# Optimization experiments

Hardware: AMD Instinct MI355X
Metric: run time of the kernel (lower is better)

## Reference

```python
import jax, jax.numpy as jnp
import numpy as np
from jax import lax

B, S, D, H, W = 4, 4096, 512, 8, 32
LL, LG = 4, 3
HD = D // H
SF = 4   # sparsity_factor
K = 7    # depthwise conv kernel


def _ln(x, g, b):
    mu = x.mean(-1, keepdims=True)
    v = ((x - mu) ** 2).mean(-1, keepdims=True)
    return (x - mu) * lax.rsqrt(v + 1e-5) * g + b


def _mha(x, wqkv, bqkv, wp, bp, bias=None):
    Bx, Sx, Dx = x.shape
    qkv = (x @ wqkv + bqkv).reshape(Bx, Sx, 3, H, HD)
    q, k, v = jnp.moveaxis(qkv, 2, 0)          # each [B,S,H,hd]
    att = jnp.einsum('bqhd,bkhd->bhqk', q, k) * (HD ** -0.5)
    if bias is not None:
        att = att + bias                        # relative position bias [1,H,W,W]
    a = jax.nn.softmax(att, axis=-1)
    o = jnp.einsum('bhqk,bkhd->bqhd', a, v).reshape(Bx, Sx, Dx)
    return o @ wp + bp


def _ffn(x, w1, b1, w2, b2):
    return jax.nn.gelu(x @ w1 + b1) @ w2 + b2


def _dwconv(x, w, b):
    # x [B,S,D], w [D,K] depthwise, 'same' padding
    y = lax.conv_general_dilated(
        x.transpose(0, 2, 1), w[:, None, :], (1,), [((K - 1) // 2, (K - 1) // 2)],
        feature_group_count=D, dimension_numbers=('NCH', 'OIH', 'NCH'))
    return (y + b[:, None]).transpose(0, 2, 1)


def _lin_interp(x, L_out):
    # torch F.interpolate(mode='linear', align_corners=False); x [B,Lin,D]
    Lin = x.shape[1]
    pos = jnp.clip((jnp.arange(L_out, dtype=jnp.float32) + 0.5) * (Lin / L_out) - 0.5,
                   0.0, Lin - 1)
    i0 = jnp.floor(pos).astype(jnp.int32)
    i1 = jnp.minimum(i0 + 1, Lin - 1)
    w = (pos - i0)[None, :, None]
    return x[:, i0] * (1.0 - w) + x[:, i1] * w


_rel_idx = np.arange(W)[:, None] - np.arange(W)[None, :] + W - 1   # [W,W]


def _local_attn(x, wqkv, bqkv, wp, bp, rel):
    # Swin-style non-overlapping window attention with relative position bias
    NW = S // W
    bias = rel[_rel_idx].transpose(2, 0, 1)[None]   # [1,H,W,W]
    xw = x.reshape(B * NW, W, D)
    return _mha(xw, wqkv, bqkv, wp, bp, bias).reshape(B, S, D)


def _global_attn(x, wqkv, bqkv, wp, bp):
    # strided sparse global attention + linear interpolation back to S
    if S > SF * 32:
        stride = max(1, S // (SF * 32))
        xs = x[:, ::stride]                         # [B, 128, D]
        return _lin_interp(_mha(xs, wqkv, bqkv, wp, bp), S)
    return _mha(x, wqkv, bqkv, wp, bp)


def _forward(x, p):
    (lqkv_w, lqkv_b, lproj_w, lproj_b, lrel, lconv_w, lconv_b,
     ln1_g, ln1_b, lffn_w1, lffn_b1, lffn_w2, lffn_b2, ln2_g, ln2_b,
     gqkv_w, gqkv_b, gproj_w, gproj_b, gn1_g, gn1_b,
     gffn_w1, gffn_b1, gffn_w2, gffn_b2, gn2_g, gn2_b,
     fw_local, fw_global, fn_g, fn_b) = p
    # local branch: window attention + depthwise conv + FFN, pre-sum/post-norm
    xl = x
    for i in range(LL):
        a = _local_attn(xl, lqkv_w[i], lqkv_b[i], lproj_w[i], lproj_b[i], lrel[i])
        xl = _ln(xl + a, ln1_g[i], ln1_b[i])
        xl = xl + _dwconv(xl, lconv_w[i], lconv_b[i])
        f = _ffn(xl, lffn_w1[i], lffn_b1[i], lffn_w2[i], lffn_b2[i])
        xl = _ln(xl + f, ln2_g[i], ln2_b[i])
    # global branch: sparse strided attention + FFN
    xg = x
    for i in range(LG):
        a = _global_attn(xg, gqkv_w[i], gqkv_b[i], gproj_w[i], gproj_b[i])
        xg = _ln(xg + a, gn1_g[i], gn1_b[i])
        f = _ffn(xg, gffn_w1[i], gffn_b1[i], gffn_w2[i], gffn_b2[i])
        xg = _ln(xg + f, gn2_g[i], gn2_b[i])
    # weighted_sum branch fusion + LayerNorm
    w = jax.nn.softmax(jnp.stack([fw_local, fw_global]))
    return _ln(w[0] * xl + w[1] * xg, fn_g, fn_b)


def setup_inputs() -> dict:
    ks = iter(jax.random.split(jax.random.key(0), 48))
    def r(shape, s=0.02):
        return jax.random.normal(next(ks), shape, dtype=jnp.float32) * s
    return {
        'x': jax.random.normal(next(ks), (B, S, D), dtype=jnp.float32),
        'lqkv_w': r((LL, D, 3 * D)), 'lqkv_b': jnp.zeros((LL, 3 * D)),
        'lproj_w': r((LL, D, D)), 'lproj_b': jnp.zeros((LL, D)),
        'lrel': r((LL, 2 * W - 1, H)),
        'lconv_w': r((LL, D, K)), 'lconv_b': jnp.zeros((LL, D)),
        'ln1_g': jnp.ones((LL, D)), 'ln1_b': jnp.zeros((LL, D)),
        'lffn_w1': r((LL, D, 4 * D)), 'lffn_b1': jnp.zeros((LL, 4 * D)),
        'lffn_w2': r((LL, 4 * D, D)), 'lffn_b2': jnp.zeros((LL, D)),
        'ln2_g': jnp.ones((LL, D)), 'ln2_b': jnp.zeros((LL, D)),
        'gqkv_w': r((LG, D, 3 * D)), 'gqkv_b': jnp.zeros((LG, 3 * D)),
        'gproj_w': r((LG, D, D)), 'gproj_b': jnp.zeros((LG, D)),
        'gn1_g': jnp.ones((LG, D)), 'gn1_b': jnp.zeros((LG, D)),
        'gffn_w1': r((LG, D, 4 * D)), 'gffn_b1': jnp.zeros((LG, 4 * D)),
        'gffn_w2': r((LG, 4 * D, D)), 'gffn_b2': jnp.zeros((LG, D)),
        'gn2_g': jnp.ones((LG, D)), 'gn2_b': jnp.zeros((LG, D)),
        'fw_local': jnp.float32(0.5), 'fw_global': jnp.float32(0.5),
        'fn_g': jnp.ones((D,)), 'fn_b': jnp.zeros((D,)),
    }


def reference(x, lqkv_w, lqkv_b, lproj_w, lproj_b, lrel, lconv_w, lconv_b,
              ln1_g, ln1_b, lffn_w1, lffn_b1, lffn_w2, lffn_b2, ln2_g, ln2_b,
              gqkv_w, gqkv_b, gproj_w, gproj_b, gn1_g, gn1_b,
              gffn_w1, gffn_b1, gffn_w2, gffn_b2, gn2_g, gn2_b,
              fw_local, fw_global, fn_g, fn_b):
    return _forward(x, (lqkv_w, lqkv_b, lproj_w, lproj_b, lrel, lconv_w, lconv_b,
                        ln1_g, ln1_b, lffn_w1, lffn_b1, lffn_w2, lffn_b2, ln2_g, ln2_b,
                        gqkv_w, gqkv_b, gproj_w, gproj_b, gn1_g, gn1_b,
                        gffn_w1, gffn_b1, gffn_w2, gffn_b2, gn2_g, gn2_b,
                        fw_local, fw_global, fn_g, fn_b))
```

## Files before the change

kernel.cpp:

```cpp
#include <hip/hip_runtime.h>
#include <hip/hip_bf16.h>
#include <math.h>

typedef __attribute__((ext_vector_type(8))) short short8;
typedef __attribute__((ext_vector_type(4))) float float4_t;
typedef __attribute__((ext_vector_type(4))) unsigned int uint4_t;
typedef __attribute__((ext_vector_type(2))) unsigned int uint2_t;

#define DEV static __device__ __forceinline__

DEV unsigned short f2b(float f) {
    union { float f; unsigned int u; } x; x.f = f;
    unsigned int r = x.u + 0x7fffu + ((x.u >> 16) & 1u);
    return (unsigned short)(r >> 16);
}
DEV float b2f(unsigned short u) {
    union { unsigned int u; float f; } x; x.u = ((unsigned int)u) << 16;
    return x.f;
}
DEV unsigned int f2b2(float lo, float hi) {
    union { __hip_bfloat162 h; unsigned int u; } c;
    c.h = __float22bfloat162_rn(make_float2(lo, hi));
    return c.u;
}
DEV float gelu_f(float x) {
    const float a = -2.3022082f, b = -0.10294372f;
    float x2 = x * x;
    float p = __builtin_fmaf(x2, b, a);
    float e = __builtin_amdgcn_exp2f(p * x);
    return x * __builtin_amdgcn_rcpf(1.0f + e);
}

DEV void gld16(unsigned short* lds, const unsigned short* g) {
    __builtin_amdgcn_global_load_lds(
        (const __attribute__((address_space(1))) unsigned int*)g,
        (__attribute__((address_space(3))) unsigned int*)lds,
        16, 0, 0);
}

__global__ __launch_bounds__(256) void transpose_cast_batch_kernel(
    const float* __restrict__ srcL, const float* __restrict__ srcG, int nl,
    unsigned short* __restrict__ dst0, size_t perL, int Kd, int Nd)
{
    const int z = blockIdx.z;
    const float* W = (z < nl) ? srcL + (size_t)z * Kd * Nd
                              : srcG + (size_t)(z - nl) * Kd * Nd;
    unsigned short* WT = dst0 + (size_t)z * perL;
    __shared__ float tile[32][33];
    int n0 = blockIdx.x * 32, k0 = blockIdx.y * 32;
    int tx = threadIdx.x & 31, ty = threadIdx.x >> 5;
    #pragma unroll
    for (int r = ty; r < 32; r += 8)
        tile[r][tx] = W[(size_t)(k0 + r) * Nd + n0 + tx];
    __syncthreads();
    #pragma unroll
    for (int r = ty; r < 32; r += 8)
        WT[(size_t)(n0 + r) * Kd + k0 + tx] = f2b(tile[tx][r]);
}

__global__ __launch_bounds__(256) void copy_cast_kernel(
    const float* __restrict__ x, float* __restrict__ xl, float* __restrict__ xg,
    unsigned short* __restrict__ xb, int n4)
{
    int i = blockIdx.x * 256 + threadIdx.x;
    if (i < n4) {
        float4_t v = ((const float4_t*)x)[i];
        ((float4_t*)xl)[i] = v;
        ((float4_t*)xg)[i] = v;
        uint2_t p = { f2b2(v[0], v[1]), f2b2(v[2], v[3]) };
        ((uint2_t*)xb)[i] = p;
    }
}

template<int BN>
__global__ __launch_bounds__(256, 3) void gemm_db_kernel(
    const unsigned short* __restrict__ A,
    const unsigned short* __restrict__ BT,
    const float* __restrict__ bias,
    const float* __restrict__ residual,
    float* __restrict__ Cf,
    unsigned short* __restrict__ Cb,
    int M, int N, int K, int act)
{
    constexpr int NI = (BN == 128) ? 4 : 2;
    __shared__ __align__(16) unsigned short As[2][128 * 32];
    __shared__ __align__(16) unsigned short Bs[2][BN * 32];
    const int tid = threadIdx.x;
    const int wave = tid >> 6, lane = tid & 63;
    const int quad = lane >> 4, l16 = lane & 15;
    const int m0 = blockIdx.x * 128, n0 = blockIdx.y * BN;
    const int wm = (BN == 128) ? (wave >> 1) * 64 : wave * 32;
    const int wn = (BN == 128) ? (wave & 1) * 64 : 0;

    float4_t acc[NI][4] = {};

    const int lrow = lane >> 2;
    const int lcol = (lane & 3) * 8;
    const int r0 = wave * 16 + lrow;
    const unsigned short* Ag0 = A  + (size_t)(m0 + r0) * K + lcol;
    const unsigned short* Ag1 = A  + (size_t)(m0 + 64 + r0) * K + lcol;
    const unsigned short* Bg0 = BT + (size_t)(n0 + r0) * K + lcol;
    const unsigned short* Bg1 = (BN == 128) ? BT + (size_t)(n0 + 64 + r0) * K + lcol : nullptr;
    const int soff = (wave * 16) * 32 + lane * 8;

    const int iters = K >> 5;
    gld16(&As[0][soff], Ag0);
    gld16(&As[0][soff + 64 * 32], Ag1);
    gld16(&Bs[0][soff], Bg0);
    if (BN == 128) gld16(&Bs[0][soff + 64 * 32], Bg1);
    __syncthreads();

    for (int k = 0; k < iters; k++) {
        const int cur = k & 1;
        if (k + 1 < iters) {
            const int koff = (k + 1) << 5;
            const int nxt = cur ^ 1;
            gld16(&As[nxt][soff], Ag0 + koff);
            gld16(&As[nxt][soff + 64 * 32], Ag1 + koff);
            gld16(&Bs[nxt][soff], Bg0 + koff);
            if (BN == 128) gld16(&Bs[nxt][soff + 64 * 32], Bg1 + koff);
        }
        short8 a[NI], b[4];
        #pragma unroll
        for (int i = 0; i < NI; i++)
            a[i] = *(const short8*)(&As[cur][(wm + i * 16 + l16) * 32 + quad * 8]);
        #pragma unroll
        for (int j = 0; j < 4; j++)
            b[j] = *(const short8*)(&Bs[cur][(wn + j * 16 + l16) * 32 + quad * 8]);
        #pragma unroll
        for (int i = 0; i < NI; i++)
            #pragma unroll
            for (int j = 0; j < 4; j++)
                acc[i][j] = __builtin_amdgcn_mfma_f32_16x16x32_bf16(b[j], a[i], acc[i][j], 0, 0, 0);
        __syncthreads();
    }

    #pragma unroll
    for (int i = 0; i < NI; i++) {
        const int row = m0 + wm + i * 16 + l16;
        #pragma unroll
        for (int j = 0; j < 4; j++) {
            const int col = n0 + wn + j * 16 + quad * 4;
            const size_t idx = (size_t)row * N + col;
            float4_t v = acc[i][j] + *(const float4_t*)(bias + col);
            if (act == 1) {
                #pragma unroll
                for (int r = 0; r < 4; r++) v[r] = gelu_f(v[r]);
            }
            if (residual) v += *(const float4_t*)(residual + idx);
            if (Cf) *(float4_t*)(Cf + idx) = v;
            if (Cb) {
                uint2_t o = { f2b2(v[0], v[1]), f2b2(v[2], v[3]) };
                *(uint2_t*)(Cb + idx) = o;
            }
        }
    }
}

__global__ __launch_bounds__(256) void ln_kernel(
    const float* __restrict__ X, const float* __restrict__ g, const float* __restrict__ b,
    float* __restrict__ Yf, unsigned short* __restrict__ Yb)
{
    const int row = blockIdx.x * 4 + (threadIdx.x >> 6);
    const int lane = threadIdx.x & 63;
    const float* xr = X + (size_t)row * 512 + lane * 8;
    float4_t v0 = *(const float4_t*)(xr);
    float4_t v1 = *(const float4_t*)(xr + 4);
    float s = v0[0] + v0[1] + v0[2] + v0[3] + v1[0] + v1[1] + v1[2] + v1[3];
    #pragma unroll
    for (int m = 32; m > 0; m >>= 1) s += __shfl_xor(s, m);
    float mu = s * (1.0f / 512.0f);
    float4_t d0 = v0 - mu, d1 = v1 - mu;
    float s2 = d0[0]*d0[0] + d0[1]*d0[1] + d0[2]*d0[2] + d0[3]*d0[3]
             + d1[0]*d1[0] + d1[1]*d1[1] + d1[2]*d1[2] + d1[3]*d1[3];
    #pragma unroll
    for (int m = 32; m > 0; m >>= 1) s2 += __shfl_xor(s2, m);
    float rs = rsqrtf(s2 * (1.0f / 512.0f) + 1e-5f);
    float4_t g0 = *(const float4_t*)(g + lane * 8);
    float4_t g1 = *(const float4_t*)(g + lane * 8 + 4);
    float4_t b0 = *(const float4_t*)(b + lane * 8);
    float4_t b1 = *(const float4_t*)(b + lane * 8 + 4);
    float4_t y0 = d0 * rs * g0 + b0;
    float4_t y1 = d1 * rs * g1 + b1;
    if (Yf) {
        float* yr = Yf + (size_t)row * 512 + lane * 8;
        *(float4_t*)(yr) = y0;
        *(float4_t*)(yr + 4) = y1;
    }
    if (Yb) {
        uint4_t pk = { f2b2(y0[0], y0[1]), f2b2(y0[2], y0[3]),
                       f2b2(y1[0], y1[1]), f2b2(y1[2], y1[3]) };
        *(uint4_t*)(Yb + (size_t)row * 512 + lane * 8) = pk;
    }
}

__global__ __launch_bounds__(256) void interp_ln_kernel(
    const float* __restrict__ GA, float* __restrict__ XG,
    const float* __restrict__ g, const float* __restrict__ b,
    unsigned short* __restrict__ Yb)
{
    const int row = blockIdx.x * 4 + (threadIdx.x >> 6);
    const int lane = threadIdx.x & 63;
    const int bb = row >> 12, sfull = row & 4095;
    float pos = (sfull + 0.5f) * (128.0f / 4096.0f) - 0.5f;
    pos = fminf(fmaxf(pos, 0.0f), 127.0f);
    int i0 = (int)floorf(pos);
    int i1 = min(i0 + 1, 127);
    float w = pos - (float)i0;
    const float* ga0 = GA + ((size_t)bb * 128 + i0) * 512 + lane * 8;
    const float* ga1 = GA + ((size_t)bb * 128 + i1) * 512 + lane * 8;
    float* xr = XG + (size_t)row * 512 + lane * 8;
    float4_t v0 = *(const float4_t*)(xr)     + *(const float4_t*)(ga0)     * (1.0f - w) + *(const float4_t*)(ga1)     * w;
    float4_t v1 = *(const float4_t*)(xr + 4) + *(const float4_t*)(ga0 + 4) * (1.0f - w) + *(const float4_t*)(ga1 + 4) * w;
    float s = v0[0] + v0[1] + v0[2] + v0[3] + v1[0] + v1[1] + v1[2] + v1[3];
    #pragma unroll
    for (int m = 32; m > 0; m >>= 1) s += __shfl_xor(s, m);
    float mu = s * (1.0f / 512.0f);
    float4_t d0 = v0 - mu, d1 = v1 - mu;
    float s2 = d0[0]*d0[0] + d0[1]*d0[1] + d0[2]*d0[2] + d0[3]*d0[3]
             + d1[0]*d1[0] + d1[1]*d1[1] + d1[2]*d1[2] + d1[3]*d1[3];
    #pragma unroll
    for (int m = 32; m > 0; m >>= 1) s2 += __shfl_xor(s2, m);
    float rs = rsqrtf(s2 * (1.0f / 512.0f) + 1e-5f);
    float4_t g0 = *(const float4_t*)(g + lane * 8);
    float4_t g1 = *(const float4_t*)(g + lane * 8 + 4);
    float4_t b0 = *(const float4_t*)(b + lane * 8);
    float4_t b1 = *(const float4_t*)(b + lane * 8 + 4);
    float4_t y0 = d0 * rs * g0 + b0;
    float4_t y1 = d1 * rs * g1 + b1;
    *(float4_t*)(xr) = y0;
    *(float4_t*)(xr + 4) = y1;
    uint4_t pk = { f2b2(y0[0], y0[1]), f2b2(y0[2], y0[3]),
                   f2b2(y1[0], y1[1]), f2b2(y1[2], y1[3]) };
    *(uint4_t*)(Yb + (size_t)row * 512 + lane * 8) = pk;
}

__global__ __launch_bounds__(256) void local_attn_kernel(
    const unsigned short* __restrict__ QKV, const float* __restrict__ rel,
    unsigned short* __restrict__ OUT)
{
    const int blk = blockIdx.x;
    const int h = blk & 7;
    const int win = (blk >> 3) & 127;
    const int b = blk >> 10;
    const int rowbase = b * 4096 + win * 32;
    __shared__ float q[32][64], k[32][65], v[32][64];
    __shared__ float sc[32][33];
    const int tid = threadIdx.x;
    const int i = tid >> 3, c = tid & 7;
    {
        const unsigned short* base = QKV + (size_t)(rowbase + i) * 1536 + h * 64 + c * 8;
        short8 qv = *(const short8*)(base);
        short8 kv = *(const short8*)(base + 512);
        short8 vv = *(const short8*)(base + 1024);
        #pragma unroll
        for (int r = 0; r < 8; r++) {
            q[i][c * 8 + r] = b2f((unsigned short)qv[r]);
            k[i][c * 8 + r] = b2f((unsigned short)kv[r]);
            v[i][c * 8 + r] = b2f((unsigned short)vv[r]);
        }
    }
    __syncthreads();
    #pragma unroll
    for (int p = 0; p < 4; p++) {
        int idx = tid + p * 256;
        int si = idx >> 5, sj = idx & 31;
        float s = 0.f;
        #pragma unroll
        for (int d = 0; d < 64; d++) s += q[si][d] * k[sj][d];
        sc[si][sj] = s * 0.125f + rel[(si - sj + 31) * 8 + h];
    }
    __syncthreads();
    {
        const int j0 = c * 4;
        float a0 = sc[i][j0], a1 = sc[i][j0 + 1], a2 = sc[i][j0 + 2], a3 = sc[i][j0 + 3];
        float mx = fmaxf(fmaxf(a0, a1), fmaxf(a2, a3));
        #pragma unroll
        for (int m = 1; m < 8; m <<= 1) mx = fmaxf(mx, __shfl_xor(mx, m));
        float e0 = __expf(a0 - mx), e1 = __expf(a1 - mx), e2 = __expf(a2 - mx), e3 = __expf(a3 - mx);
        float sum = e0 + e1 + e2 + e3;
        #pragma unroll
        for (int m = 1; m < 8; m <<= 1) sum += __shfl_xor(sum, m);
        float inv = 1.0f / sum;
        sc[i][j0] = e0 * inv; sc[i][j0 + 1] = e1 * inv; sc[i][j0 + 2] = e2 * inv; sc[i][j0 + 3] = e3 * inv;
    }
    __syncthreads();
    float o[8] = {};
    #pragma unroll
    for (int j = 0; j < 32; j++) {
        float a = sc[i][j];
        #pragma unroll
        for (int r = 0; r < 8; r++) o[r] += a * v[j][c * 8 + r];
    }
    uint4_t pk = { f2b2(o[0], o[1]), f2b2(o[2], o[3]), f2b2(o[4], o[5]), f2b2(o[6], o[7]) };
    *(uint4_t*)(OUT + (size_t)(rowbase + i) * 512 + h * 64 + c * 8) = pk;
}

__global__ __launch_bounds__(256) void gather_xs_kernel(
    const float* __restrict__ XG, unsigned short* __restrict__ XSB)
{
    int i = blockIdx.x * 256 + threadIdx.x;
    if (i < 65536) {
        int dv = (i & 127) * 4, t = (i >> 7) & 127, b = i >> 14;
        float4_t v = *(const float4_t*)(XG + ((size_t)b * 4096 + t * 32) * 512 + dv);
        uint2_t p = { f2b2(v[0], v[1]), f2b2(v[2], v[3]) };
        *(uint2_t*)(XSB + (size_t)i * 4) = p;
    }
}

__global__ __launch_bounds__(256) void global_attn_kernel(
    const unsigned short* __restrict__ GQKV, unsigned short* __restrict__ GOUT)
{
    const int blk = blockIdx.x;
    const int qt = blk & 3, h = (blk >> 2) & 7, b = blk >> 5;
    __shared__ unsigned short ks[128 * 64], vs[128 * 64];
    __shared__ float qs[32 * 64];
    __shared__ float sc[32 * 128];
    const int tid = threadIdx.x;
    for (int idx = tid; idx < 128 * 64; idx += 256) {
        int j = idx >> 6, d = idx & 63;
        const unsigned short* rowp = GQKV + (size_t)(b * 128 + j) * 1536 + h * 64 + d;
        ks[idx] = rowp[512];
        vs[idx] = rowp[1024];
    }
    for (int idx = tid; idx < 32 * 64; idx += 256) {
        int i = idx >> 6, d = idx & 63;
        qs[idx] = b2f(GQKV[(size_t)(b * 128 + qt * 32 + i) * 1536 + h * 64 + d]);
    }
    __syncthreads();
    for (int idx = tid; idx < 32 * 128; idx += 256) {
        int i = idx >> 7, j = idx & 127;
        float s = 0.f;
        #pragma unroll
        for (int d = 0; d < 64; d++) s += qs[i * 64 + d] * b2f(ks[j * 64 + d]);
        sc[idx] = s * 0.125f;
    }
    __syncthreads();
    if (tid < 32) {
        float mx = -1e30f;
        for (int j = 0; j < 128; j++) mx = fmaxf(mx, sc[tid * 128 + j]);
        float sum = 0.f;
        for (int j = 0; j < 128; j++) { float e = __expf(sc[tid * 128 + j] - mx); sc[tid * 128 + j] = e; sum += e; }
        float inv = 1.0f / sum;
        for (int j = 0; j < 128; j++) sc[tid * 128 + j] *= inv;
    }
    __syncthreads();
    for (int idx = tid; idx < 32 * 64; idx += 256) {
        int i = idx >> 6, d = idx & 63;
        float o = 0.f;
        for (int j = 0; j < 128; j++) o += sc[i * 128 + j] * b2f(vs[j * 64 + d]);
        GOUT[(size_t)(b * 128 + qt * 32 + i) * 512 + h * 64 + d] = f2b(o);
    }
}

__global__ __launch_bounds__(256) void dwconv_add_kernel(
    const float* __restrict__ X, const float* __restrict__ wconv, const float* __restrict__ bconv,
    float* __restrict__ Yf, unsigned short* __restrict__ Yb)
{
    __shared__ float wT[7][512];
    const int tid = threadIdx.x;
    for (int idx = tid; idx < 3584; idx += 256) {
        int d = idx / 7, t = idx - d * 7;
        wT[t][d] = wconv[idx];
    }
    __syncthreads();
    const int b = blockIdx.y;
    const int s0 = blockIdx.x * 16 + (tid >> 7) * 8;
    const int dv = (tid & 127) * 4;
    const float* Xb = X + ((size_t)b * 4096) * 512 + dv;

    float4_t win[14];
    #pragma unroll
    for (int j = 0; j < 14; j++) {
        int ss = s0 - 3 + j;
        win[j] = (ss >= 0 && ss < 4096) ? *(const float4_t*)(Xb + (size_t)ss * 512)
                                        : (float4_t){0.f, 0.f, 0.f, 0.f};
    }
    float4_t bias = *(const float4_t*)(bconv + dv);
    float4_t w[7];
    #pragma unroll
    for (int t = 0; t < 7; t++) w[t] = *(const float4_t*)(&wT[t][dv]);

    #pragma unroll
    for (int j = 0; j < 8; j++) {
        float4_t acc = bias;
        #pragma unroll
        for (int t = 0; t < 7; t++) acc += win[j + t] * w[t];
        float4_t v = win[j + 3] + acc;
        size_t e = ((size_t)b * 4096 + s0 + j) * 512 + dv;
        *(float4_t*)(Yf + e) = v;
        uint2_t o = { f2b2(v[0], v[1]), f2b2(v[2], v[3]) };
        *(uint2_t*)(Yb + e) = o;
    }
}

__global__ __launch_bounds__(256) void final_kernel(
    const float* __restrict__ XL, const float* __restrict__ XG,
    const float* __restrict__ fwl, const float* __restrict__ fwg,
    const float* __restrict__ g, const float* __restrict__ bb, float* __restrict__ out)
{
    const int row = blockIdx.x * 4 + (threadIdx.x >> 6);
    const int lane = threadIdx.x & 63;
    float a = fwl[0], cc = fwg[0];
    float m = fmaxf(a, cc);
    float ea = __expf(a - m), ec = __expf(cc - m);
    float w0 = ea / (ea + ec), w1 = ec / (ea + ec);
    const float* xlr = XL + (size_t)row * 512 + lane * 8;
    const float* xgr = XG + (size_t)row * 512 + lane * 8;
    float4_t v0 = *(const float4_t*)(xlr)     * w0 + *(const float4_t*)(xgr)     * w1;
    float4_t v1 = *(const float4_t*)(xlr + 4) * w0 + *(const float4_t*)(xgr + 4) * w1;
    float s = v0[0] + v0[1] + v0[2] + v0[3] + v1[0] + v1[1] + v1[2] + v1[3];
    #pragma unroll
    for (int mm = 32; mm > 0; mm >>= 1) s += __shfl_xor(s, mm);
    float mu = s * (1.0f / 512.0f);
    float4_t d0 = v0 - mu, d1 = v1 - mu;
    float s2 = d0[0]*d0[0] + d0[1]*d0[1] + d0[2]*d0[2] + d0[3]*d0[3]
             + d1[0]*d1[0] + d1[1]*d1[1] + d1[2]*d1[2] + d1[3]*d1[3];
    #pragma unroll
    for (int mm = 32; mm > 0; mm >>= 1) s2 += __shfl_xor(s2, mm);
    float rs = rsqrtf(s2 * (1.0f / 512.0f) + 1e-5f);
    float4_t g0 = *(const float4_t*)(g + lane * 8);
    float4_t g1 = *(const float4_t*)(g + lane * 8 + 4);
    float4_t b0 = *(const float4_t*)(bb + lane * 8);
    float4_t b1 = *(const float4_t*)(bb + lane * 8 + 4);
    float* orow = out + (size_t)row * 512 + lane * 8;
    *(float4_t*)(orow)     = d0 * rs * g0 + b0;
    *(float4_t*)(orow + 4) = d1 * rs * g1 + b1;
}

extern "C" void kernel_launch(void* const* d_in, const int* in_sizes, int n_in,
                              void* d_out, int out_size, void* d_ws, size_t ws_size,
                              hipStream_t stream)
{
    (void)in_sizes; (void)n_in; (void)out_size; (void)ws_size;
    const float* x       = (const float*)d_in[0];
    const float* lqkv_w  = (const float*)d_in[1];
    const float* lqkv_b  = (const float*)d_in[2];
    const float* lproj_w = (const float*)d_in[3];
    const float* lproj_b = (const float*)d_in[4];
    const float* lrel    = (const float*)d_in[5];
    const float* lconv_w = (const float*)d_in[6];
    const float* lconv_b = (const float*)d_in[7];
    const float* ln1_g   = (const float*)d_in[8];
    const float* ln1_b   = (const float*)d_in[9];
    const float* lffn_w1 = (const float*)d_in[10];
    const float* lffn_b1 = (const float*)d_in[11];
    const float* lffn_w2 = (const float*)d_in[12];
    const float* lffn_b2 = (const float*)d_in[13];
    const float* ln2_g   = (const float*)d_in[14];
    const float* ln2_b   = (const float*)d_in[15];
    const float* gqkv_w  = (const float*)d_in[16];
    const float* gqkv_b  = (const float*)d_in[17];
    const float* gproj_w = (const float*)d_in[18];
    const float* gproj_b = (const float*)d_in[19];
    const float* gn1_g   = (const float*)d_in[20];
    const float* gn1_b   = (const float*)d_in[21];
    const float* gffn_w1 = (const float*)d_in[22];
    const float* gffn_b1 = (const float*)d_in[23];
    const float* gffn_w2 = (const float*)d_in[24];
    const float* gffn_b2 = (const float*)d_in[25];
    const float* gn2_g   = (const float*)d_in[26];
    const float* gn2_b   = (const float*)d_in[27];
    const float* fw_local  = (const float*)d_in[28];
    const float* fw_global = (const float*)d_in[29];
    const float* fn_g    = (const float*)d_in[30];
    const float* fn_b    = (const float*)d_in[31];
    float* out = (float*)d_out;

    const int Btot = 4 * 4096;
    const int nel = Btot * 512;

    char* wsb = (char*)d_ws;
    size_t off = 0;
    auto alloc = [&](size_t bytes) -> void* {
        void* p = wsb + off;
        off = (off + bytes + 255) & ~(size_t)255;
        return p;
    };
    float*          XL   = (float*)alloc((size_t)nel * 4);
    float*          XG   = (float*)alloc((size_t)nel * 4);
    float*          TMP  = (float*)alloc((size_t)nel * 4);
    unsigned short* XBl  = (unsigned short*)alloc((size_t)nel * 2);
    unsigned short* XBg  = (unsigned short*)alloc((size_t)nel * 2);
    unsigned short* AOUT = (unsigned short*)alloc((size_t)nel * 2);
    unsigned short* BIG  = (unsigned short*)alloc((size_t)Btot * 2048 * 2);
    unsigned short* WT   = (unsigned short*)alloc((size_t)22020096 * 2);
    unsigned short* XSB  = (unsigned short*)alloc((size_t)512 * 512 * 2);
    unsigned short* GQKV = (unsigned short*)alloc((size_t)512 * 1536 * 2);
    unsigned short* GOUT = (unsigned short*)alloc((size_t)512 * 512 * 2);
    float*          GA   = (float*)alloc((size_t)512 * 512 * 4);

    const size_t perL = 3145728;
    {
        dim3 blk(256);
        transpose_cast_batch_kernel<<<dim3(1536/32, 512/32, 7), blk, 0, stream>>>(
            lqkv_w, gqkv_w, 4, WT, perL, 512, 1536);
        transpose_cast_batch_kernel<<<dim3(512/32, 512/32, 7), blk, 0, stream>>>(
            lproj_w, gproj_w, 4, WT + 786432, perL, 512, 512);
        transpose_cast_batch_kernel<<<dim3(2048/32, 512/32, 7), blk, 0, stream>>>(
            lffn_w1, gffn_w1, 4, WT + 786432 + 262144, perL, 512, 2048);
        transpose_cast_batch_kernel<<<dim3(512/32, 2048/32, 7), blk, 0, stream>>>(
            lffn_w2, gffn_w2, 4, WT + 786432 + 262144 + 1048576, perL, 2048, 512);
    }

    copy_cast_kernel<<<dim3(nel / 1024), dim3(256), 0, stream>>>(x, XL, XG, XBl, nel / 4);

    auto gemm = [&](const unsigned short* A_, const unsigned short* BT_, const float* bias_,
                    const float* res_, float* Cf_, unsigned short* Cb_,
                    int M_, int N_, int K_, int act_) {
        if (N_ >= 1024) {
            dim3 g(M_ / 128, N_ / 128);
            gemm_db_kernel<128><<<g, dim3(256), 0, stream>>>(A_, BT_, bias_, res_, Cf_, Cb_, M_, N_, K_, act_);
        } else {
            dim3 g(M_ / 128, N_ / 64);
            gemm_db_kernel<64><<<g, dim3(256), 0, stream>>>(A_, BT_, bias_, res_, Cf_, Cb_, M_, N_, K_, act_);
        }
    };

    for (int i = 0; i < 4; i++) {
        unsigned short* base  = WT + (size_t)i * perL;
        unsigned short* qkvT  = base;
        unsigned short* projT = base + 786432;
        unsigned short* w1T   = base + 786432 + 262144;
        unsigned short* w2T   = base + 786432 + 262144 + 1048576;

        gemm(XBl, qkvT, lqkv_b + i * 1536, nullptr, nullptr, BIG, Btot, 1536, 512, 0);
        local_attn_kernel<<<dim3(4096), dim3(256), 0, stream>>>(BIG, lrel + (size_t)i * 63 * 8, AOUT);
        gemm(AOUT, projT, lproj_b + i * 512, XL, TMP, nullptr, Btot, 512, 512, 0);
        ln_kernel<<<dim3(Btot / 4), dim3(256), 0, stream>>>(TMP, ln1_g + i * 512, ln1_b + i * 512, XL, (unsigned short*)nullptr);
        dwconv_add_kernel<<<dim3(256, 4), dim3(256), 0, stream>>>(XL, lconv_w + (size_t)i * 512 * 7, lconv_b + i * 512, TMP, XBl);
        gemm(XBl, w1T, lffn_b1 + i * 2048, nullptr, nullptr, BIG, Btot, 2048, 512, 1);
        gemm(BIG, w2T, lffn_b2 + i * 512, TMP, TMP, nullptr, Btot, 512, 2048, 0);
        ln_kernel<<<dim3(Btot / 4), dim3(256), 0, stream>>>(TMP, ln2_g + i * 512, ln2_b + i * 512, XL, XBl);
    }

    for (int i = 0; i < 3; i++) {
        unsigned short* base  = WT + (size_t)(4 + i) * perL;
        unsigned short* qkvT  = base;
        unsigned short* projT = base + 786432;
        unsigned short* w1T   = base + 786432 + 262144;
        unsigned short* w2T   = base + 786432 + 262144 + 1048576;

        gather_xs_kernel<<<dim3(256), dim3(256), 0, stream>>>(XG, XSB);
        gemm(XSB, qkvT, gqkv_b + i * 1536, nullptr, nullptr, GQKV, 512, 1536, 512, 0);
        global_attn_kernel<<<dim3(128), dim3(256), 0, stream>>>(GQKV, GOUT);
        gemm(GOUT, projT, gproj_b + i * 512, nullptr, GA, nullptr, 512, 512, 512, 0);
        interp_ln_kernel<<<dim3(Btot / 4), dim3(256), 0, stream>>>(GA, XG, gn1_g + i * 512, gn1_b + i * 512, XBg);
        gemm(XBg, w1T, gffn_b1 + i * 2048, nullptr, nullptr, BIG, Btot, 2048, 512, 1);
        gemm(BIG, w2T, gffn_b2 + i * 512, XG, TMP, nullptr, Btot, 512, 2048, 0);
        ln_kernel<<<dim3(Btot / 4), dim3(256), 0, stream>>>(TMP, gn2_g + i * 512, gn2_b + i * 512, XG, XBg);
    }

    final_kernel<<<dim3(Btot / 4), dim3(256), 0, stream>>>(XL, XG, fw_local, fw_global, fn_g, fn_b, out);
}
```

Measured before the change: 1.943 ms.

## Add 512-thread 256-row GEMM with interleaved LDS/MFMA phases and prefetch

Adds a new bf16 MFMA GEMM kernel with 256xBN block tiles and 8 waves. Each K step is split into four phases that interleave LDS fragment reads, MFMA quarters and asynchronous global-to-LDS staging for step t+2, using explicit vmcnt/lgkmcnt waits, barriers and setprio. The dispatcher sends the large-M GEMMs to this kernel. The goal is to raise per-block data reuse and overlap memory traffic with matrix math. The cost is heavier register and LDS use (about 128KB LDS, acc 8xNJ) and many barriers that may limit occupancy.

```diff
diff --git a/kernel.cpp b/kernel.cpp
--- a/kernel.cpp
+++ b/kernel.cpp
@@ -156,6 +156,160 @@
         }
     }
 }
+
+
+#define BAR __builtin_amdgcn_s_barrier()
+#define LGKM0 asm volatile("s_waitcnt lgkmcnt(0)" ::: "memory")
+#define VMC8 asm volatile("s_waitcnt vmcnt(8)" ::: "memory")
+#define VMC6 asm volatile("s_waitcnt vmcnt(6)" ::: "memory")
+#define VMC0 asm volatile("s_waitcnt vmcnt(0)" ::: "memory")
+#define VMLP do { if constexpr (BN == 256) { VMC8; } else { VMC6; } } while (0)
+
+#define DSA(d, rh) do { \
+    const unsigned short* s_ = &AS[d][wm][0]; \
+    _Pragma("unroll") \
+    for (int ii = 0; ii < 4; ++ii) { \
+        const int row_ = ((rh) * 4 + ii) * 16 + l16; \
+        const int sw_ = (row_ & 7) << 3; \
+        a[ii][0] = *(const short8*)(s_ + row_ * 64 + ((quad * 8) ^ sw_)); \
+        a[ii][1] = *(const short8*)(s_ + row_ * 64 + ((32 + quad * 8) ^ sw_)); \
+    } } while (0)
+
+#define DSB(d, ch) do { \
+    const unsigned short* s_ = &BS[d][wn >> 1][0]; \
+    _Pragma("unroll") \
+    for (int jj = 0; jj < NJH; ++jj) { \
+        const int row_ = wnb + ((ch) * NJH + jj) * 16 + l16; \
+        const int sw_ = (row_ & 7) << 3; \
+        b[(ch) * NJH + jj][0] = *(const short8*)(s_ + row_ * 64 + ((quad * 8) ^ sw_)); \
+        b[(ch) * NJH + jj][1] = *(const short8*)(s_ + row_ * 64 + ((32 + quad * 8) ^ sw_)); \
+    } } while (0)
+
+#define MFMAQ(rh, ch) do { \
+    __builtin_amdgcn_s_setprio(1); \
+    _Pragma("unroll") \
+    for (int ii = 0; ii < 4; ++ii) { \
+        _Pragma("unroll") \
+        for (int jj = 0; jj < NJH; ++jj) { \
+            acc[(rh)*4+ii][(ch)*NJH+jj] = __builtin_amdgcn_mfma_f32_16x16x32_bf16( \
+                b[(ch)*NJH+jj][0], a[ii][0], acc[(rh)*4+ii][(ch)*NJH+jj], 0, 0, 0); \
+            acc[(rh)*4+ii][(ch)*NJH+jj] = __builtin_amdgcn_mfma_f32_16x16x32_bf16( \
+                b[(ch)*NJH+jj][1], a[ii][1], acc[(rh)*4+ii][(ch)*NJH+jj], 0, 0, 0); \
+        } } \
+    __builtin_amdgcn_s_setprio(0); } while (0)
+
+#define KSTEP(d, t, DOSTAGE, VMOP) do { \
+     \
+    DSA(d, 0); DSB(d, 0); BAR; LGKM0; MFMAQ(0, 0); BAR; \
+     \
+    DSB(d, 1); BAR; LGKM0; MFMAQ(0, 1); BAR; \
+     \
+    DSA(d, 1); if (DOSTAGE) { stageB(d, (t) + 2); } BAR; LGKM0; MFMAQ(1, 0); BAR; \
+     \
+    if (DOSTAGE) { stageA(d, (t) + 2); } VMOP; BAR; MFMAQ(1, 1); BAR; \
+  } while (0)
+
+template<int BN>
+__global__ __launch_bounds__(512, 2) void gemm_8ph_kernel(
+    const unsigned short* __restrict__ A,
+    const unsigned short* __restrict__ BT,
+    const float* __restrict__ bias,
+    const float* __restrict__ residual,
+    float* __restrict__ Cf,
+    unsigned short* __restrict__ Cb,
+    int M, int N, int K, int act)
+{
+    static_assert(BN == 256 || BN == 128, "BN");
+    constexpr int NJ  = BN / 64;
+    constexpr int NJH = NJ / 2;
+    constexpr int HB  = BN / 2;
+    constexpr int BLH = (BN == 256) ? 2 : 1;
+
+    __shared__ __align__(16) unsigned short AS[2][2][128 * 64];
+    __shared__ __align__(16) unsigned short BS[2][2][HB * 64];
+
+    const int tid = threadIdx.x;
+    const int wave = tid >> 6, lane = tid & 63;
+    const int quad = lane >> 4, l16 = lane & 15;
+    const int wm = wave >> 2;
+    const int wn = wave & 3;
+    const int m0 = blockIdx.x * 256, n0 = blockIdx.y * BN;
+    const int wnb = (wn & 1) * (BN / 4);
+
+    const int trow = tid >> 3;
+    const int xo = (((tid & 7) ^ (trow & 7)) << 3);
+
+    const unsigned short* gA[2][2];
+    #pragma unroll
+    for (int h = 0; h < 2; ++h)
+        #pragma unroll
+        for (int l = 0; l < 2; ++l)
+            gA[h][l] = A + (size_t)(m0 + h * 128 + l * 64 + trow) * K + xo;
+    const unsigned short* gB[2][BLH];
+    #pragma unroll
+    for (int h = 0; h < 2; ++h)
+        #pragma unroll
+        for (int l = 0; l < BLH; ++l)
+            gB[h][l] = BT + (size_t)(n0 + h * HB + l * 64 + trow) * K + xo;
+
+    auto stageA = [&](int d, int t) {
+        #pragma unroll
+        for (int h = 0; h < 2; ++h)
+            #pragma unroll
+            for (int l = 0; l < 2; ++l)
+                gld16(&AS[d][h][l * 4096 + tid * 8], gA[h][l] + t * 64);
+    };
+    auto stageB = [&](int d, int t) {
+        #pragma unroll
+        for (int h = 0; h < 2; ++h)
+            #pragma unroll
+            for (int l = 0; l < BLH; ++l)
+                gld16(&BS[d][h][l * 4096 + tid * 8], gB[h][l] + t * 64);
+    };
+
+    short8 a[4][2];
+    short8 b[NJ][2];
+    float4_t acc[8][NJ] = {};
+
+    const int T = K >> 6;
+
+    stageA(0, 0); stageB(0, 0);
+    stageA(1, 1); stageB(1, 1);
+    VMLP; BAR;
+
+    for (int t = 0; t < T - 2; ++t) {
+        const int d = t & 1;
+        KSTEP(d, t, true, VMLP);
+    }
+    KSTEP((T - 2) & 1, T - 2, false, VMC0);
+    KSTEP((T - 1) & 1, T - 1, false, (void)0);
+
+    #pragma unroll
+    for (int i = 0; i < 8; ++i) {
+        const int row = m0 + wm * 128 + i * 16 + l16;
+        #pragma unroll
+        for (int j = 0; j < NJ; ++j) {
+            const int col = n0 + (wn >> 1) * HB + wnb + j * 16 + quad * 4;
+            const size_t idx = (size_t)row * N + col;
+            float4_t v = acc[i][j] + *(const float4_t*)(bias + col);
+            if (act == 1) {
+                #pragma unroll
+                for (int r = 0; r < 4; r++) v[r] = gelu_f(v[r]);
+            }
+            if (residual) v += *(const float4_t*)(residual + idx);
+            if (Cf) *(float4_t*)(Cf + idx) = v;
+            if (Cb) {
+                uint2_t o = { f2b2(v[0], v[1]), f2b2(v[2], v[3]) };
+                *(uint2_t*)(Cb + idx) = o;
+            }
+        }
+    }
+}
+
+#undef KSTEP
+#undef MFMAQ
+#undef DSB
+#undef DSA
 
 __global__ __launch_bounds__(256) void ln_kernel(
     const float* __restrict__ X, const float* __restrict__ g, const float* __restrict__ b,
@@ -508,7 +662,15 @@
     auto gemm = [&](const unsigned short* A_, const unsigned short* BT_, const float* bias_,
                     const float* res_, float* Cf_, unsigned short* Cb_,
                     int M_, int N_, int K_, int act_) {
-        if (N_ >= 1024) {
+        if (M_ >= 1024 && (M_ % 256) == 0 && (K_ % 128) == 0 && (N_ % 128) == 0) {
+            if ((N_ % 256) == 0 && N_ >= 1536) {
+                dim3 g(M_ / 256, N_ / 256);
+                gemm_8ph_kernel<256><<<g, dim3(512), 0, stream>>>(A_, BT_, bias_, res_, Cf_, Cb_, M_, N_, K_, act_);
+            } else {
+                dim3 g(M_ / 256, N_ / 128);
+                gemm_8ph_kernel<128><<<g, dim3(512), 0, stream>>>(A_, BT_, bias_, res_, Cf_, Cb_, M_, N_, K_, act_);
+            }
+        } else if (N_ >= 1024) {
             dim3 g(M_ / 128, N_ / 128);
             gemm_db_kernel<128><<<g, dim3(256), 0, stream>>>(A_, BT_, bias_, res_, Cf_, Cb_, M_, N_, K_, act_);
         } else {
```

After: 1.919 ms. No clear change (-1.2%).
